# Kernel optimization log

Measured on AMD Instinct MI355X. Metric: run time of the kernel, lower is better.

The kernel has to match this reference:

```python
import jax, jax.numpy as jnp
import numpy as np

B, S, H, E, K = 4, 4096, 1024, 8, 2


def setup_inputs() -> dict:
    key = jax.random.key(0)
    ks = jax.random.split(key, 5)
    scale = 1.0 / np.sqrt(H)
    return {
        "x": jax.random.normal(ks[0], (B, S, H), dtype=jnp.float32),
        "gate_w": jax.random.normal(ks[1], (H, E), dtype=jnp.float32) * scale,
        "gate_b": jnp.zeros((E,), dtype=jnp.float32),
        "expert_w": jax.random.normal(ks[2], (E, H, H), dtype=jnp.float32) * scale,
        "expert_b": jnp.zeros((E, H), dtype=jnp.float32),
    }


def reference(x, gate_w, gate_b, expert_w, expert_b):
    bsz, seq_len, hsz = x.shape
    h = x.reshape(-1, hsz)                              # [T, H], T = B*S

    # --- router ---
    router_logits = h @ gate_w + gate_b                 # [T, E]
    probs = jax.nn.softmax(router_logits, axis=-1)
    top_w, top_idx = jax.lax.top_k(probs, K)            # [T, K]
    top_w = top_w / jnp.sum(top_w, axis=-1, keepdims=True)

    # combine weight per (token, expert): sum over top-k slots of w * onehot(idx)
    one_hot = jax.nn.one_hot(top_idx, E, dtype=h.dtype)  # [T, K, E]
    combine = jnp.einsum("tk,tke->te", top_w, one_hot)   # [T, E]

    # --- experts (dense grouped GEMM, masked-combined; same math as gather/scatter loop) ---
    expert_out = jnp.einsum("th,ehd->etd", h, expert_w) + expert_b[:, None, :]  # [E, T, H]
    out = jnp.einsum("te,etd->td", combine, expert_out)                          # [T, H]

    return out.reshape(bsz, seq_len, hsz), router_logits
```

## Files before the change

kernel.cpp:

```cpp
#include <hip/hip_runtime.h>

#define TT 16384
#define HH 1024
#define EE 8

typedef __attribute__((ext_vector_type(8))) short short8;
typedef __attribute__((ext_vector_type(4))) float f32x4;

__device__ inline unsigned short f2bf(float f) {
    union { float f; unsigned int u; } v; v.f = f;
    unsigned int u = v.u;
    unsigned int r = (u + 0x7FFFu + ((u >> 16) & 1u)) >> 16;
    return (unsigned short)r;
}

__global__ __launch_bounds__(256) void transpose_w_kernel(
    const float* __restrict__ w, unsigned short* __restrict__ wt)
{
    __shared__ unsigned short tile[64][66];
    int bid = blockIdx.x;
    int e   = bid >> 8;
    int rem = bid & 255;
    int hb  = ((rem >> 4) & 15) * 64;
    int db  = (rem & 15) * 64;
    int tid = threadIdx.x;
    int c4  = (tid & 15) * 4;
    int r0  = tid >> 4;

    const float* we = w + (size_t)e * HH * HH;
    #pragma unroll
    for (int i = 0; i < 4; ++i) {
        int r = i * 16 + r0;
        float4 v = *(const float4*)(we + (size_t)(hb + r) * HH + db + c4);
        tile[r][c4 + 0] = f2bf(v.x);
        tile[r][c4 + 1] = f2bf(v.y);
        tile[r][c4 + 2] = f2bf(v.z);
        tile[r][c4 + 3] = f2bf(v.w);
    }
    __syncthreads();
    unsigned short* wte = wt + (size_t)e * HH * HH;
    #pragma unroll
    for (int i = 0; i < 4; ++i) {
        int dr = i * 16 + r0;
        ushort4 o;
        o.x = tile[c4 + 0][dr];
        o.y = tile[c4 + 1][dr];
        o.z = tile[c4 + 2][dr];
        o.w = tile[c4 + 3][dr];
        *(ushort4*)(wte + (size_t)(db + dr) * HH + hb + c4) = o;
    }
}

__global__ __launch_bounds__(256) void router_decide_kernel(
    const float* __restrict__ x, const float* __restrict__ gw,
    const float* __restrict__ gb, const float* __restrict__ eb,
    float* __restrict__ out, float* __restrict__ logits,
    unsigned short* __restrict__ xb, int* __restrict__ tops_i,
    float* __restrict__ tops_w)
{
    __shared__ float gwt[EE][HH];
    int tid = threadIdx.x;
    for (int i = tid; i < (HH * EE) / 4; i += 256) {
        float4 v = ((const float4*)gw)[i];
        int b4 = i * 4;
        gwt[(b4 + 0) & 7][(b4 + 0) >> 3] = v.x;
        gwt[(b4 + 1) & 7][(b4 + 1) >> 3] = v.y;
        gwt[(b4 + 2) & 7][(b4 + 2) >> 3] = v.z;
        gwt[(b4 + 3) & 7][(b4 + 3) >> 3] = v.w;
    }
    __syncthreads();

    const int lane = tid & 63;
    const int wv   = tid >> 6;

    for (int tk = 0; tk < 4; ++tk) {
        const int t = blockIdx.x * 16 + wv * 4 + tk;
        const float* xrow = x + (size_t)t * HH;
        unsigned short* xbrow = xb + (size_t)t * HH;

        float acc[8];
        #pragma unroll
        for (int e = 0; e < 8; ++e) acc[e] = 0.0f;

        #pragma unroll
        for (int i = 0; i < 4; ++i) {
            int idx = i * 256 + lane * 4;
            float4 v = *(const float4*)(xrow + idx);
            ushort4 bv;
            bv.x = f2bf(v.x); bv.y = f2bf(v.y); bv.z = f2bf(v.z); bv.w = f2bf(v.w);
            *(ushort4*)(xbrow + idx) = bv;
            #pragma unroll
            for (int e = 0; e < 8; ++e) {
                float4 g = *(const float4*)(&gwt[e][idx]);
                acc[e] += v.x * g.x + v.y * g.y + v.z * g.z + v.w * g.w;
            }
        }
        #pragma unroll
        for (int e = 0; e < 8; ++e) {
            #pragma unroll
            for (int off = 32; off >= 1; off >>= 1)
                acc[e] += __shfl_xor(acc[e], off, 64);
        }
        float lg[8];
        #pragma unroll
        for (int e = 0; e < 8; ++e) lg[e] = acc[e] + gb[e];

        float myv = 0.0f;
        #pragma unroll
        for (int e = 0; e < 8; ++e) myv = (lane == e) ? lg[e] : myv;
        if (lane < 8) logits[(size_t)t * EE + lane] = myv;

        int i0 = 0;
        #pragma unroll
        for (int e = 1; e < 8; ++e) if (lg[e] > lg[i0]) i0 = e;
        int i1 = (i0 == 0) ? 1 : 0;
        #pragma unroll
        for (int e = 0; e < 8; ++e) if (e != i0 && lg[e] > lg[i1]) i1 = e;

        float w0 = 1.0f / (1.0f + expf(lg[i1] - lg[i0]));
        float w1 = 1.0f - w0;

        if (lane == 0) {
            tops_i[t] = i0 | (i1 << 3);
            tops_w[t] = w0;
        }

        const float* b0 = eb + (size_t)i0 * HH;
        const float* b1 = eb + (size_t)i1 * HH;
        float* orow = out + (size_t)t * HH;
        #pragma unroll
        for (int i = 0; i < 4; ++i) {
            int idx = i * 256 + lane * 4;
            float4 a = *(const float4*)(b0 + idx);
            float4 c = *(const float4*)(b1 + idx);
            float4 r;
            r.x = w0 * a.x + w1 * c.x;
            r.y = w0 * a.y + w1 * c.y;
            r.z = w0 * a.z + w1 * c.z;
            r.w = w0 * a.w + w1 * c.w;
            *(float4*)(orow + idx) = r;
        }
    }
}

__global__ __launch_bounds__(256) void build_lists_kernel(
    const int* __restrict__ tops_i, const float* __restrict__ tops_w,
    int* __restrict__ counts, int* __restrict__ tokl, float* __restrict__ wl)
{
    __shared__ int lcnt[EE];
    __shared__ int gbase[EE];
    int tid = threadIdx.x;
    if (tid < EE) lcnt[tid] = 0;
    __syncthreads();

    int t   = blockIdx.x * 256 + tid;
    int rec = tops_i[t];
    int i0  = rec & 7;
    int i1  = (rec >> 3) & 7;
    float w0 = tops_w[t];
    float w1 = 1.0f - w0;

    int r0 = atomicAdd(&lcnt[i0], 1);
    int r1 = atomicAdd(&lcnt[i1], 1);
    __syncthreads();

    if (tid < EE) gbase[tid] = atomicAdd(&counts[tid], lcnt[tid]);
    __syncthreads();

    int p0 = gbase[i0] + r0;
    tokl[i0 * TT + p0] = t; wl[i0 * TT + p0] = w0;
    int p1 = gbase[i1] + r1;
    tokl[i1 * TT + p1] = t; wl[i1 * TT + p1] = w1;
}

#define BM 128
#define BN 128
#define BK 64

__global__ __launch_bounds__(256) void moe_gemm_kernel(
    const unsigned short* __restrict__ xb, const unsigned short* __restrict__ wt,
    const int* __restrict__ counts, const int* __restrict__ tokl,
    const float* __restrict__ wl, float* __restrict__ out)
{
    int bid = blockIdx.x;
    int e   = bid & 7;
    int j   = bid >> 3;
    int mb  = j >> 3;
    int nb  = j & 7;
    int cnt = counts[e];
    int row0 = mb * BM;
    if (row0 >= cnt) return;

    __shared__ __align__(16) unsigned short Alds[BM * BK];
    __shared__ __align__(16) unsigned short Blds[BN * BK];
    __shared__ int   toks[BM];
    __shared__ float wgts[BM];

    int tid = threadIdx.x;
    if (tid < BM) {
        int g = row0 + tid;
        bool ok = g < cnt;
        toks[tid] = ok ? tokl[e * TT + g] : 0;
        wgts[tid] = ok ? wl[e * TT + g] : 0.0f;
    }
    __syncthreads();

    const int lane = tid & 63;
    const int wv   = tid >> 6;
    const int wr   = wv >> 1, wc = wv & 1;
    const int mrow = wr * 64, ncol = wc * 64;

    f32x4 acc[4][4];
    #pragma unroll
    for (int m = 0; m < 4; ++m)
        #pragma unroll
        for (int n = 0; n < 4; ++n) acc[m][n] = (f32x4)0.0f;

    const unsigned short* wte = wt + (size_t)e * HH * HH + (size_t)(nb * BN) * HH;
    const int off = wv * 1024 + lane * 16;

    for (int kt = 0; kt < HH / BK; ++kt) {
        int k0 = kt * BK;
        #pragma unroll
        for (int rnd = 0; rnd < 4; ++rnd) {
            int o  = rnd * 4096 + off;
            int r  = o >> 7;
            int cb = o & 127;
            const unsigned short* srcA = xb + (size_t)toks[r] * HH + k0 + (cb >> 1);
            __builtin_amdgcn_global_load_lds(
                (const __attribute__((address_space(1))) void*)srcA,
                (__attribute__((address_space(3))) void*)((char*)Alds + rnd * 4096 + wv * 1024),
                16, 0, 0);
            const unsigned short* srcB = wte + (size_t)r * HH + k0 + (cb >> 1);
            __builtin_amdgcn_global_load_lds(
                (const __attribute__((address_space(1))) void*)srcB,
                (__attribute__((address_space(3))) void*)((char*)Blds + rnd * 4096 + wv * 1024),
                16, 0, 0);
        }
        __syncthreads();
        #pragma unroll
        for (int kk = 0; kk < 2; ++kk) {
            int kb = kk * 64 + (lane >> 4) * 16;
            short8 av[4], bv[4];
            #pragma unroll
            for (int m = 0; m < 4; ++m)
                av[m] = *(const short8*)((const char*)Alds + (mrow + m * 16 + (lane & 15)) * 128 + kb);
            #pragma unroll
            for (int n = 0; n < 4; ++n)
                bv[n] = *(const short8*)((const char*)Blds + (ncol + n * 16 + (lane & 15)) * 128 + kb);
            #pragma unroll
            for (int m = 0; m < 4; ++m)
                #pragma unroll
                for (int n = 0; n < 4; ++n)
                    acc[m][n] = __builtin_amdgcn_mfma_f32_16x16x32_bf16(av[m], bv[n], acc[m][n], 0, 0, 0);
        }
        __syncthreads();
    }

    #pragma unroll
    for (int m = 0; m < 4; ++m) {
        int lr0 = mrow + m * 16 + ((lane >> 4) << 2);
        #pragma unroll
        for (int rg = 0; rg < 4; ++rg) {
            int lr = lr0 + rg;
            int tkn = toks[lr];
            float wg = wgts[lr];
            if (wg != 0.0f) {
                float* orow = out + (size_t)tkn * HH + nb * BN + ncol + (lane & 15);
                #pragma unroll
                for (int n = 0; n < 4; ++n)
                    atomicAdd(orow + n * 16, wg * acc[m][n][rg]);
            }
        }
    }
}

extern "C" void kernel_launch(void* const* d_in, const int* in_sizes, int n_in,
                              void* d_out, int out_size, void* d_ws, size_t ws_size,
                              hipStream_t stream) {
    const float* x  = (const float*)d_in[0];
    const float* gw = (const float*)d_in[1];
    const float* gb = (const float*)d_in[2];
    const float* ew = (const float*)d_in[3];
    const float* eb = (const float*)d_in[4];
    float* out    = (float*)d_out;
    float* logits = out + (size_t)TT * HH;

    char* w = (char*)d_ws;
    unsigned short* xb = (unsigned short*)w;
    unsigned short* wt = (unsigned short*)(w + (size_t)TT * HH * 2);
    char* p  = w + (size_t)TT * HH * 2 + (size_t)EE * HH * HH * 2;
    int*   counts = (int*)p;
    int*   tokl   = (int*)(p + 256);
    float* wl     = (float*)(p + 256 + (size_t)EE * TT * 4);
    int*   tops_i = (int*)(p + 256 + 2 * (size_t)EE * TT * 4);
    float* tops_w = (float*)(p + 256 + 2 * (size_t)EE * TT * 4 + TT * 4);

    hipMemsetAsync(counts, 0, 256, stream);
    hipLaunchKernelGGL(transpose_w_kernel, dim3(EE * 256), dim3(256), 0, stream, ew, wt);
    hipLaunchKernelGGL(router_decide_kernel, dim3(TT / 16), dim3(256), 0, stream,
                       x, gw, gb, eb, out, logits, xb, tops_i, tops_w);
    hipLaunchKernelGGL(build_lists_kernel, dim3(TT / 256), dim3(256), 0, stream,
                       tops_i, tops_w, counts, tokl, wl);
    hipLaunchKernelGGL(moe_gemm_kernel, dim3(EE * (TT / BM) * (HH / BN)), dim3(256), 0, stream,
                       xb, wt, counts, tokl, wl, out);
}
```

Before: 323.1 us.

## Double-buffer LDS in MoE GEMM and widen router blocks to 512 threads

The grouped GEMM now keeps two LDS buffers for A and B, so the async global-to-LDS loads for the next K tile are issued before the MFMA work on the current tile. This is meant to hide global load latency behind compute, at the cost of twice the LDS per block, which may lower occupancy. The per-row gather addresses are also hoisted out of the K loop. The router kernel moves to 512 threads per block with 2 tokens per wave instead of 4, giving it more parallelism for the same grid.

```diff
diff --git a/kernel.cpp b/kernel.cpp
--- a/kernel.cpp
+++ b/kernel.cpp
@@ -51,7 +51,7 @@
     }
 }
 
-__global__ __launch_bounds__(256) void router_decide_kernel(
+__global__ __launch_bounds__(512) void router_decide_kernel(
     const float* __restrict__ x, const float* __restrict__ gw,
     const float* __restrict__ gb, const float* __restrict__ eb,
     float* __restrict__ out, float* __restrict__ logits,
@@ -60,7 +60,7 @@
 {
     __shared__ float gwt[EE][HH];
     int tid = threadIdx.x;
-    for (int i = tid; i < (HH * EE) / 4; i += 256) {
+    for (int i = tid; i < (HH * EE) / 4; i += 512) {
         float4 v = ((const float4*)gw)[i];
         int b4 = i * 4;
         gwt[(b4 + 0) & 7][(b4 + 0) >> 3] = v.x;
@@ -73,8 +73,9 @@
     const int lane = tid & 63;
     const int wv   = tid >> 6;
 
-    for (int tk = 0; tk < 4; ++tk) {
-        const int t = blockIdx.x * 16 + wv * 4 + tk;
+    #pragma unroll
+    for (int tk = 0; tk < 2; ++tk) {
+        const int t = blockIdx.x * 16 + wv * 2 + tk;
         const float* xrow = x + (size_t)t * HH;
         unsigned short* xbrow = xb + (size_t)t * HH;
 
@@ -191,8 +192,8 @@
     int row0 = mb * BM;
     if (row0 >= cnt) return;
 
-    __shared__ __align__(16) unsigned short Alds[BM * BK];
-    __shared__ __align__(16) unsigned short Blds[BN * BK];
+    __shared__ __align__(16) unsigned short Alds[2][BM * BK];
+    __shared__ __align__(16) unsigned short Blds[2][BN * BK];
     __shared__ int   toks[BM];
     __shared__ float wgts[BM];
 
@@ -219,43 +220,70 @@
     const unsigned short* wte = wt + (size_t)e * HH * HH + (size_t)(nb * BN) * HH;
     const int off = wv * 1024 + lane * 16;
 
-    for (int kt = 0; kt < HH / BK; ++kt) {
-        int k0 = kt * BK;
-        #pragma unroll
-        for (int rnd = 0; rnd < 4; ++rnd) {
-            int o  = rnd * 4096 + off;
-            int r  = o >> 7;
-            int cb = o & 127;
-            const unsigned short* srcA = xb + (size_t)toks[r] * HH + k0 + (cb >> 1);
-            __builtin_amdgcn_global_load_lds(
-                (const __attribute__((address_space(1))) void*)srcA,
-                (__attribute__((address_space(3))) void*)((char*)Alds + rnd * 4096 + wv * 1024),
-                16, 0, 0);
-            const unsigned short* srcB = wte + (size_t)r * HH + k0 + (cb >> 1);
-            __builtin_amdgcn_global_load_lds(
-                (const __attribute__((address_space(1))) void*)srcB,
-                (__attribute__((address_space(3))) void*)((char*)Blds + rnd * 4096 + wv * 1024),
-                16, 0, 0);
-        }
+    const unsigned short* abase[4];
+    const unsigned short* bbase[4];
+    #pragma unroll
+    for (int rnd = 0; rnd < 4; ++rnd) {
+        int o  = rnd * 4096 + off;
+        int r  = o >> 7;
+        int cb = (o & 127) >> 1;
+        abase[rnd] = xb + (size_t)toks[r] * HH + cb;
+        bbase[rnd] = wte + (size_t)r * HH + cb;
+    }
+
+#define STAGE(buf, k0)                                                         \
+    {                                                                          \
+        _Pragma("unroll")                                                      \
+        for (int rnd = 0; rnd < 4; ++rnd) {                                    \
+            __builtin_amdgcn_global_load_lds(                                  \
+                (const __attribute__((address_space(1))) void*)(abase[rnd] + (k0)), \
+                (__attribute__((address_space(3))) void*)((char*)&Alds[buf][0] + rnd * 4096 + wv * 1024), \
+                16, 0, 0);                                                     \
+            __builtin_amdgcn_global_load_lds(                                  \
+                (const __attribute__((address_space(1))) void*)(bbase[rnd] + (k0)), \
+                (__attribute__((address_space(3))) void*)((char*)&Blds[buf][0] + rnd * 4096 + wv * 1024), \
+                16, 0, 0);                                                     \
+        }                                                                      \
+    }
+
+#define COMPUTE(buf)                                                           \
+    {                                                                          \
+        _Pragma("unroll")                                                      \
+        for (int kk = 0; kk < 2; ++kk) {                                       \
+            int kb = kk * 64 + (lane >> 4) * 16;                               \
+            short8 av[4], bv[4];                                               \
+            _Pragma("unroll")                                                  \
+            for (int m = 0; m < 4; ++m)                                        \
+                av[m] = *(const short8*)((const char*)&Alds[buf][0] + (mrow + m * 16 + (lane & 15)) * 128 + kb); \
+            _Pragma("unroll")                                                  \
+            for (int n = 0; n < 4; ++n)                                        \
+                bv[n] = *(const short8*)((const char*)&Blds[buf][0] + (ncol + n * 16 + (lane & 15)) * 128 + kb); \
+            _Pragma("unroll")                                                  \
+            for (int m = 0; m < 4; ++m)                                        \
+                _Pragma("unroll")                                              \
+                for (int n = 0; n < 4; ++n)                                    \
+                    acc[m][n] = __builtin_amdgcn_mfma_f32_16x16x32_bf16(av[m], bv[n], acc[m][n], 0, 0, 0); \
+        }                                                                      \
+    }
+
+    STAGE(0, 0);
+    __syncthreads();
+
+    for (int kt = 0; kt < 14; kt += 2) {
+        STAGE(1, (kt + 1) * BK);
+        COMPUTE(0);
         __syncthreads();
-        #pragma unroll
-        for (int kk = 0; kk < 2; ++kk) {
-            int kb = kk * 64 + (lane >> 4) * 16;
-            short8 av[4], bv[4];
-            #pragma unroll
-            for (int m = 0; m < 4; ++m)
-                av[m] = *(const short8*)((const char*)Alds + (mrow + m * 16 + (lane & 15)) * 128 + kb);
-            #pragma unroll
-            for (int n = 0; n < 4; ++n)
-                bv[n] = *(const short8*)((const char*)Blds + (ncol + n * 16 + (lane & 15)) * 128 + kb);
-            #pragma unroll
-            for (int m = 0; m < 4; ++m)
-                #pragma unroll
-                for (int n = 0; n < 4; ++n)
-                    acc[m][n] = __builtin_amdgcn_mfma_f32_16x16x32_bf16(av[m], bv[n], acc[m][n], 0, 0, 0);
-        }
+        STAGE(0, (kt + 2) * BK);
+        COMPUTE(1);
         __syncthreads();
     }
+    STAGE(1, 15 * BK);
+    COMPUTE(0);
+    __syncthreads();
+    COMPUTE(1);
+
+#undef STAGE
+#undef COMPUTE
 
     #pragma unroll
     for (int m = 0; m < 4; ++m) {
@@ -298,7 +326,7 @@
 
     hipMemsetAsync(counts, 0, 256, stream);
     hipLaunchKernelGGL(transpose_w_kernel, dim3(EE * 256), dim3(256), 0, stream, ew, wt);
-    hipLaunchKernelGGL(router_decide_kernel, dim3(TT / 16), dim3(256), 0, stream,
+    hipLaunchKernelGGL(router_decide_kernel, dim3(TT / 16), dim3(512), 0, stream,
                        x, gw, gb, eb, out, logits, xb, tops_i, tops_w);
     hipLaunchKernelGGL(build_lists_kernel, dim3(TT / 256), dim3(256), 0, stream,
                        tops_i, tops_w, counts, tokl, wl);
```

After: 359.4 us. 11.2% more time.

## Split router into logits-only kernel plus grid-stride bf16-cast/bias-init kernel

Applied to the files above, without the earlier changes.

The fused router kernel is split into two kernels. The first does only the logits and top-2 selection, one token per wave, with all four x loads issued up front. A new grid-stride kernel then does the bf16 cast of x and the bias-combine initialisation of the output. The goal is more memory-level parallelism for the streaming work, which previously ran serially per wave, at the cost of an extra launch and reading x twice. The GEMM also hoists per-round gather base addresses out of its k-loop.

```diff
diff --git a/kernel.cpp b/kernel.cpp
--- a/kernel.cpp
+++ b/kernel.cpp
@@ -51,12 +51,10 @@
     }
 }
 
-__global__ __launch_bounds__(256) void router_decide_kernel(
+__global__ __launch_bounds__(256) void router_logits_kernel(
     const float* __restrict__ x, const float* __restrict__ gw,
-    const float* __restrict__ gb, const float* __restrict__ eb,
-    float* __restrict__ out, float* __restrict__ logits,
-    unsigned short* __restrict__ xb, int* __restrict__ tops_i,
-    float* __restrict__ tops_w)
+    const float* __restrict__ gb, float* __restrict__ logits,
+    int* __restrict__ tops_i, float* __restrict__ tops_w)
 {
     __shared__ float gwt[EE][HH];
     int tid = threadIdx.x;
@@ -72,74 +70,53 @@
 
     const int lane = tid & 63;
     const int wv   = tid >> 6;
-
-    for (int tk = 0; tk < 4; ++tk) {
-        const int t = blockIdx.x * 16 + wv * 4 + tk;
-        const float* xrow = x + (size_t)t * HH;
-        unsigned short* xbrow = xb + (size_t)t * HH;
-
-        float acc[8];
-        #pragma unroll
-        for (int e = 0; e < 8; ++e) acc[e] = 0.0f;
-
-        #pragma unroll
-        for (int i = 0; i < 4; ++i) {
-            int idx = i * 256 + lane * 4;
-            float4 v = *(const float4*)(xrow + idx);
-            ushort4 bv;
-            bv.x = f2bf(v.x); bv.y = f2bf(v.y); bv.z = f2bf(v.z); bv.w = f2bf(v.w);
-            *(ushort4*)(xbrow + idx) = bv;
-            #pragma unroll
-            for (int e = 0; e < 8; ++e) {
-                float4 g = *(const float4*)(&gwt[e][idx]);
-                acc[e] += v.x * g.x + v.y * g.y + v.z * g.z + v.w * g.w;
-            }
-        }
-        #pragma unroll
-        for (int e = 0; e < 8; ++e) {
-            #pragma unroll
-            for (int off = 32; off >= 1; off >>= 1)
-                acc[e] += __shfl_xor(acc[e], off, 64);
-        }
-        float lg[8];
-        #pragma unroll
-        for (int e = 0; e < 8; ++e) lg[e] = acc[e] + gb[e];
-
-        float myv = 0.0f;
-        #pragma unroll
-        for (int e = 0; e < 8; ++e) myv = (lane == e) ? lg[e] : myv;
-        if (lane < 8) logits[(size_t)t * EE + lane] = myv;
-
-        int i0 = 0;
-        #pragma unroll
-        for (int e = 1; e < 8; ++e) if (lg[e] > lg[i0]) i0 = e;
-        int i1 = (i0 == 0) ? 1 : 0;
-        #pragma unroll
-        for (int e = 0; e < 8; ++e) if (e != i0 && lg[e] > lg[i1]) i1 = e;
-
-        float w0 = 1.0f / (1.0f + expf(lg[i1] - lg[i0]));
-        float w1 = 1.0f - w0;
-
-        if (lane == 0) {
-            tops_i[t] = i0 | (i1 << 3);
-            tops_w[t] = w0;
-        }
-
-        const float* b0 = eb + (size_t)i0 * HH;
-        const float* b1 = eb + (size_t)i1 * HH;
-        float* orow = out + (size_t)t * HH;
-        #pragma unroll
-        for (int i = 0; i < 4; ++i) {
-            int idx = i * 256 + lane * 4;
-            float4 a = *(const float4*)(b0 + idx);
-            float4 c = *(const float4*)(b1 + idx);
-            float4 r;
-            r.x = w0 * a.x + w1 * c.x;
-            r.y = w0 * a.y + w1 * c.y;
-            r.z = w0 * a.z + w1 * c.z;
-            r.w = w0 * a.w + w1 * c.w;
-            *(float4*)(orow + idx) = r;
-        }
+    const int t    = blockIdx.x * 4 + wv;
+    const float* xrow = x + (size_t)t * HH;
+
+    float4 v0 = *(const float4*)(xrow + 0 * 256 + lane * 4);
+    float4 v1 = *(const float4*)(xrow + 1 * 256 + lane * 4);
+    float4 v2 = *(const float4*)(xrow + 2 * 256 + lane * 4);
+    float4 v3 = *(const float4*)(xrow + 3 * 256 + lane * 4);
+
+    float acc[8];
+    #pragma unroll
+    for (int e = 0; e < 8; ++e) {
+        float4 g0 = *(const float4*)(&gwt[e][0 * 256 + lane * 4]);
+        float4 g1 = *(const float4*)(&gwt[e][1 * 256 + lane * 4]);
+        float4 g2 = *(const float4*)(&gwt[e][2 * 256 + lane * 4]);
+        float4 g3 = *(const float4*)(&gwt[e][3 * 256 + lane * 4]);
+        acc[e] = v0.x * g0.x + v0.y * g0.y + v0.z * g0.z + v0.w * g0.w
+               + v1.x * g1.x + v1.y * g1.y + v1.z * g1.z + v1.w * g1.w
+               + v2.x * g2.x + v2.y * g2.y + v2.z * g2.z + v2.w * g2.w
+               + v3.x * g3.x + v3.y * g3.y + v3.z * g3.z + v3.w * g3.w;
+    }
+    #pragma unroll
+    for (int e = 0; e < 8; ++e) {
+        #pragma unroll
+        for (int off = 32; off >= 1; off >>= 1)
+            acc[e] += __shfl_xor(acc[e], off, 64);
+    }
+    float lg[8];
+    #pragma unroll
+    for (int e = 0; e < 8; ++e) lg[e] = acc[e] + gb[e];
+
+    float myv = 0.0f;
+    #pragma unroll
+    for (int e = 0; e < 8; ++e) myv = (lane == e) ? lg[e] : myv;
+    if (lane < 8) logits[(size_t)t * EE + lane] = myv;
+
+    int i0 = 0;
+    #pragma unroll
+    for (int e = 1; e < 8; ++e) if (lg[e] > lg[i0]) i0 = e;
+    int i1 = (i0 == 0) ? 1 : 0;
+    #pragma unroll
+    for (int e = 0; e < 8; ++e) if (e != i0 && lg[e] > lg[i1]) i1 = e;
+
+    float w0 = 1.0f / (1.0f + expf(lg[i1] - lg[i0]));
+
+    if (lane == 0) {
+        tops_i[t] = i0 | (i1 << 3);
+        tops_w[t] = w0;
     }
 }
 
@@ -171,6 +148,38 @@
     tokl[i0 * TT + p0] = t; wl[i0 * TT + p0] = w0;
     int p1 = gbase[i1] + r1;
     tokl[i1 * TT + p1] = t; wl[i1 * TT + p1] = w1;
+}
+
+__global__ __launch_bounds__(256) void stream_init_kernel(
+    const float* __restrict__ x, const float* __restrict__ eb,
+    const int* __restrict__ tops_i, const float* __restrict__ tops_w,
+    unsigned short* __restrict__ xb, float* __restrict__ out)
+{
+    const int N4 = TT * HH / 4;
+    int stride = gridDim.x * 256;
+    for (int f = blockIdx.x * 256 + threadIdx.x; f < N4; f += stride) {
+        int t  = f >> 8;
+        int c4 = f & 255;
+        int rec = tops_i[t];
+        int i0  = rec & 7;
+        int i1  = (rec >> 3) & 7;
+        float w0 = tops_w[t];
+        float w1 = 1.0f - w0;
+
+        float4 v = ((const float4*)x)[f];
+        ushort4 bv;
+        bv.x = f2bf(v.x); bv.y = f2bf(v.y); bv.z = f2bf(v.z); bv.w = f2bf(v.w);
+        ((ushort4*)xb)[f] = bv;
+
+        float4 a = *(const float4*)(eb + (size_t)i0 * HH + c4 * 4);
+        float4 c = *(const float4*)(eb + (size_t)i1 * HH + c4 * 4);
+        float4 r;
+        r.x = w0 * a.x + w1 * c.x;
+        r.y = w0 * a.y + w1 * c.y;
+        r.z = w0 * a.z + w1 * c.z;
+        r.w = w0 * a.w + w1 * c.w;
+        ((float4*)out)[f] = r;
+    }
 }
 
 #define BM 128
@@ -219,21 +228,27 @@
     const unsigned short* wte = wt + (size_t)e * HH * HH + (size_t)(nb * BN) * HH;
     const int off = wv * 1024 + lane * 16;
 
+    const unsigned short* abase[4];
+    const unsigned short* bbase[4];
+    #pragma unroll
+    for (int rnd = 0; rnd < 4; ++rnd) {
+        int o  = rnd * 4096 + off;
+        int r  = o >> 7;
+        int cb = (o & 127) >> 1;
+        abase[rnd] = xb + (size_t)toks[r] * HH + cb;
+        bbase[rnd] = wte + (size_t)r * HH + cb;
+    }
+
     for (int kt = 0; kt < HH / BK; ++kt) {
         int k0 = kt * BK;
         #pragma unroll
         for (int rnd = 0; rnd < 4; ++rnd) {
-            int o  = rnd * 4096 + off;
-            int r  = o >> 7;
-            int cb = o & 127;
-            const unsigned short* srcA = xb + (size_t)toks[r] * HH + k0 + (cb >> 1);
             __builtin_amdgcn_global_load_lds(
-                (const __attribute__((address_space(1))) void*)srcA,
+                (const __attribute__((address_space(1))) void*)(abase[rnd] + k0),
                 (__attribute__((address_space(3))) void*)((char*)Alds + rnd * 4096 + wv * 1024),
                 16, 0, 0);
-            const unsigned short* srcB = wte + (size_t)r * HH + k0 + (cb >> 1);
             __builtin_amdgcn_global_load_lds(
-                (const __attribute__((address_space(1))) void*)srcB,
+                (const __attribute__((address_space(1))) void*)(bbase[rnd] + k0),
                 (__attribute__((address_space(3))) void*)((char*)Blds + rnd * 4096 + wv * 1024),
                 16, 0, 0);
         }
@@ -298,10 +313,12 @@
 
     hipMemsetAsync(counts, 0, 256, stream);
     hipLaunchKernelGGL(transpose_w_kernel, dim3(EE * 256), dim3(256), 0, stream, ew, wt);
-    hipLaunchKernelGGL(router_decide_kernel, dim3(TT / 16), dim3(256), 0, stream,
-                       x, gw, gb, eb, out, logits, xb, tops_i, tops_w);
+    hipLaunchKernelGGL(router_logits_kernel, dim3(TT / 4), dim3(256), 0, stream,
+                       x, gw, gb, logits, tops_i, tops_w);
     hipLaunchKernelGGL(build_lists_kernel, dim3(TT / 256), dim3(256), 0, stream,
                        tops_i, tops_w, counts, tokl, wl);
+    hipLaunchKernelGGL(stream_init_kernel, dim3(2048), dim3(256), 0, stream,
+                       x, eb, tops_i, tops_w, xb, out);
     hipLaunchKernelGGL(moe_gemm_kernel, dim3(EE * (TT / BM) * (HH / BN)), dim3(256), 0, stream,
                        xb, wt, counts, tokl, wl, out);
 }
```

After: 364.3 us. 1.13x slower.
